# Kernel tuning notes

Hardware: AMD Instinct MI355X
Metric: run time of the kernel (lower is better)

The kernel has to match this reference:

```python
import jax, jax.numpy as jnp
import numpy as np

B, T, C, H = 2, 2048, 1024, 16


def setup_inputs() -> dict:
    key = jax.random.key(0)
    ks = jax.random.split(key, 9)
    s = 1.0 / np.sqrt(C)
    return {
        "query": jax.random.normal(ks[0], (B, T, C), dtype=jnp.float32),
        "Wq": jax.random.normal(ks[1], (C, C), dtype=jnp.float32) * s,
        "bq": jnp.zeros((C,), dtype=jnp.float32),
        "Wk": jax.random.normal(ks[2], (C, C), dtype=jnp.float32) * s,
        "bk": jnp.zeros((C,), dtype=jnp.float32),
        "Wv": jax.random.normal(ks[3], (C, C), dtype=jnp.float32) * s,
        "bv": jnp.zeros((C,), dtype=jnp.float32),
        "Wp": jax.random.normal(ks[4], (C, C), dtype=jnp.float32) * s,
        "bp": jnp.zeros((C,), dtype=jnp.float32),
        "n_head": H,
    }


def reference(query, Wq, bq, Wk, bk, Wv, bv, Wp, bp, n_head):
    b, t, c = query.shape
    d = c // n_head
    # QKV projections -> [b, h, t, d]
    q = (query @ Wq + bq).reshape(b, t, n_head, d).transpose(0, 2, 1, 3)
    k = (query @ Wk + bk).reshape(b, t, n_head, d).transpose(0, 2, 1, 3)
    v = (query @ Wv + bv).reshape(b, t, n_head, d).transpose(0, 2, 1, 3)
    scale = 1.0 / jnp.sqrt(jnp.asarray(d, dtype=query.dtype))
    att = jnp.einsum('bhtd,bhsd->bhts', q, k) * scale  # [b,h,t,t]
    causal = jnp.tril(jnp.ones((t, t), dtype=bool))
    att = jnp.where(causal[None, None, :, :], att, -jnp.inf)
    att = jax.nn.softmax(att, axis=-1)
    y = jnp.einsum('bhts,bhsd->bhtd', att, v)  # [b,h,t,d]
    y = y.transpose(0, 2, 1, 3).reshape(b, t, c)
    return y @ Wp + bp
```

## Files before the change

kernel.cpp:

```cpp
#include <hip/hip_runtime.h>
#include <math.h>

#define B_ 2
#define T_ 2048
#define C_ 1024
#define H_ 16
#define D_ 64
#define M_ (B_*T_)

typedef __bf16 bf16x8 __attribute__((ext_vector_type(8)));
typedef __bf16 bf16x4 __attribute__((ext_vector_type(4)));
typedef float  f32x4  __attribute__((ext_vector_type(4)));

__device__ __forceinline__ unsigned short f2bf(float f) {
    unsigned int u = __float_as_uint(f);
    u += 0x7FFFu + ((u >> 16) & 1u);
    return (unsigned short)(u >> 16);
}

__device__ __forceinline__ void gload16(const void* g, void* l) {
    __builtin_amdgcn_global_load_lds(
        (const __attribute__((address_space(1))) void*)g,
        (__attribute__((address_space(3))) void*)l, 16, 0, 0);
}

__global__ __launch_bounds__(256) void prep_kernel(
    const float* __restrict__ X, unsigned short* __restrict__ Xb,
    const float* __restrict__ W0, const float* __restrict__ W1,
    const float* __restrict__ W2, const float* __restrict__ W3,
    unsigned short* __restrict__ T0, unsigned short* __restrict__ T1,
    unsigned short* __restrict__ T2, unsigned short* __restrict__ T3)
{
    const int tid = threadIdx.x;
    if (blockIdx.x < 2048) {
        const size_t i = ((size_t)blockIdx.x * 256 + tid) * 8;
        const float4 a = *(const float4*)&X[i];
        const float4 b = *(const float4*)&X[i + 4];
        ushort4 s0, s1;
        s0.x = f2bf(a.x); s0.y = f2bf(a.y); s0.z = f2bf(a.z); s0.w = f2bf(a.w);
        s1.x = f2bf(b.x); s1.y = f2bf(b.y); s1.z = f2bf(b.z); s1.w = f2bf(b.w);
        *(ushort4*)&Xb[i]     = s0;
        *(ushort4*)&Xb[i + 4] = s1;
        return;
    }
    const int bz = blockIdx.x - 2048;
    const int z = bz >> 10, rem = bz & 1023;
    const float* W; unsigned short* Wt;
    switch (z) {
        case 0: W = W0; Wt = T0; break;
        case 1: W = W1; Wt = T1; break;
        case 2: W = W2; Wt = T2; break;
        default: W = W3; Wt = T3; break;
    }
    __shared__ unsigned short tile[32][33];
    const int k0 = (rem >> 5) * 32, n0 = (rem & 31) * 32;
    {
        const int r = tid >> 3, c = (tid & 7) * 4;
        const float4 v = *(const float4*)&W[(size_t)(k0 + r)*C_ + n0 + c];
        tile[c+0][r] = f2bf(v.x);
        tile[c+1][r] = f2bf(v.y);
        tile[c+2][r] = f2bf(v.z);
        tile[c+3][r] = f2bf(v.w);
    }
    __syncthreads();
    {
        const int r = tid >> 3, c = (tid & 7) * 4;
        ushort4 s;
        s.x = tile[r][c+0]; s.y = tile[r][c+1]; s.z = tile[r][c+2]; s.w = tile[r][c+3];
        *(ushort4*)&Wt[(size_t)(n0 + r)*C_ + k0 + c] = s;
    }
}

__global__ __launch_bounds__(256) void gemm_proj_kernel(
    const unsigned short* __restrict__ A, const unsigned short* __restrict__ Bt,
    const float* __restrict__ bias, float* __restrict__ out)
{
    __shared__ __align__(16) unsigned short Als[2][64 * 32];
    __shared__ __align__(16) unsigned short Bls[2][128 * 32];

    const int tid  = threadIdx.x;
    const int lane = tid & 63;
    const int wave = tid >> 6;
    const int wm = wave >> 1, wn = wave & 1;
    const int l15 = lane & 15, quad = lane >> 4;
    const int m0 = blockIdx.y * 64, n0 = blockIdx.x * 128;
    const int srow = lane >> 2;
    const int scol = (lane & 3) * 8;

    const f32x4 zero4 = {0.f, 0.f, 0.f, 0.f};
    f32x4 acc[2][4];
    #pragma unroll
    for (int i = 0; i < 2; ++i)
        #pragma unroll
        for (int j = 0; j < 4; ++j) acc[i][j] = zero4;

    for (int k0 = 0; k0 < C_; k0 += 64) {
        __syncthreads();
        #pragma unroll
        for (int h = 0; h < 2; ++h) {
            gload16(&A[(size_t)(m0 + wave*16 + srow)*C_ + k0 + h*32 + scol],
                    &Als[h][(wave*16)*32]);
            #pragma unroll
            for (int u = 0; u < 2; ++u) {
                const int r = wave*32 + u*16 + srow;
                gload16(&Bt[(size_t)(n0 + r)*C_ + k0 + h*32 + scol],
                        &Bls[h][(wave*32 + u*16)*32]);
            }
        }
        __syncthreads();

        #pragma unroll
        for (int h = 0; h < 2; ++h) {
            bf16x8 af[2], bfr[4];
            #pragma unroll
            for (int i = 0; i < 2; ++i)
                af[i] = *(const bf16x8*)&Als[h][(wm*32 + i*16 + l15)*32 + quad*8];
            #pragma unroll
            for (int j = 0; j < 4; ++j)
                bfr[j] = *(const bf16x8*)&Bls[h][(wn*64 + j*16 + l15)*32 + quad*8];

            #pragma unroll
            for (int i = 0; i < 2; ++i)
                #pragma unroll
                for (int j = 0; j < 4; ++j)
                    acc[i][j] = __builtin_amdgcn_mfma_f32_16x16x32_bf16(
                        af[i], bfr[j], acc[i][j], 0, 0, 0);
        }
    }

    #pragma unroll
    for (int j = 0; j < 4; ++j) {
        const int n = n0 + wn*64 + j*16 + l15;
        const float bv = bias[n];
        #pragma unroll
        for (int i = 0; i < 2; ++i)
            #pragma unroll
            for (int r = 0; r < 4; ++r) {
                const int m = m0 + wm*32 + i*16 + quad*4 + r;
                out[(size_t)m*C_ + n] = acc[i][j][r] + bv;
            }
    }
}

__global__ __launch_bounds__(512, 2) void gemm256_qkv_kernel(
    const unsigned short* __restrict__ A, const unsigned short* __restrict__ Bt,
    const float* __restrict__ b0, const float* __restrict__ b1,
    const float* __restrict__ b2,
    unsigned short* __restrict__ outq, unsigned short* __restrict__ outk,
    unsigned short* __restrict__ outv)
{
    __shared__ __align__(16) unsigned short lds[4 * 16384];

    const int tid  = threadIdx.x;
    const int lane = tid & 63;
    const int wave = tid >> 6;
    const int l15  = lane & 15, quad = lane >> 4;
    const int wm   = wave >> 2, wn = wave & 3;
    const int m0   = blockIdx.y * 256, n0 = blockIdx.x * 256;

    const int lrow = lane >> 2;
    const int csw  = ((lane & 3) ^ ((lane >> 3) & 3)) * 8;
    const int sw8  = (quad ^ ((l15 >> 1) & 3)) * 8;

#define STAGE(tt) do {                                                         \
        const int bi_ = ((tt) & 3) << 14;                                      \
        const int k0_ = (tt) << 5;                                             \
        const int ra_ = m0 + wave*32 + lrow;                                   \
        const int rb_ = n0 + wave*32 + lrow;                                   \
        gload16(&A [(size_t)ra_*C_ + k0_ + csw],      &lds[bi_ + wave*1024]);  \
        gload16(&Bt[(size_t)rb_*C_ + k0_ + csw],      &lds[bi_ + 8192 + wave*1024]); \
        gload16(&A [(size_t)(ra_+16)*C_ + k0_ + csw], &lds[bi_ + wave*1024 + 512]);  \
        gload16(&Bt[(size_t)(rb_+16)*C_ + k0_ + csw], &lds[bi_ + 8192 + wave*1024 + 512]); \
    } while (0)

    const f32x4 zero4 = {0.f, 0.f, 0.f, 0.f};
    f32x4 acc[8][4];
    #pragma unroll
    for (int i = 0; i < 8; ++i)
        #pragma unroll
        for (int j = 0; j < 4; ++j) acc[i][j] = zero4;

    STAGE(0); STAGE(1); STAGE(2);

    for (int t = 0; t < 32; ++t) {
        const int bi = (t & 3) << 14;
        __builtin_amdgcn_s_barrier();
        __builtin_amdgcn_sched_barrier(0);
        if (t < 29) {
            STAGE(t + 3);
            asm volatile("s_waitcnt vmcnt(12)" ::: "memory");
        } else if (t == 29) {
            asm volatile("s_waitcnt vmcnt(8)" ::: "memory");
        } else if (t == 30) {
            asm volatile("s_waitcnt vmcnt(4)" ::: "memory");
        } else {
            asm volatile("s_waitcnt vmcnt(0)" ::: "memory");
        }
        __builtin_amdgcn_s_barrier();
        __builtin_amdgcn_sched_barrier(0);

        const unsigned short* Ab = &lds[bi];
        const unsigned short* Bb = &lds[bi + 8192];

        bf16x8 bfr[4], af[4];
        #pragma unroll
        for (int j = 0; j < 4; ++j)
            bfr[j] = *(const bf16x8*)&Bb[(wn*64 + j*16 + l15)*32 + sw8];
        #pragma unroll
        for (int i = 0; i < 4; ++i)
            af[i] = *(const bf16x8*)&Ab[(wm*128 + i*16 + l15)*32 + sw8];

        __builtin_amdgcn_s_setprio(1);
        #pragma unroll
        for (int i = 0; i < 4; ++i)
            #pragma unroll
            for (int j = 0; j < 4; ++j)
                acc[i][j] = __builtin_amdgcn_mfma_f32_16x16x32_bf16(
                    af[i], bfr[j], acc[i][j], 0, 0, 0);
        __builtin_amdgcn_s_setprio(0);

        #pragma unroll
        for (int i = 0; i < 4; ++i)
            af[i] = *(const bf16x8*)&Ab[(wm*128 + 64 + i*16 + l15)*32 + sw8];

        __builtin_amdgcn_s_setprio(1);
        #pragma unroll
        for (int i = 0; i < 4; ++i)
            #pragma unroll
            for (int j = 0; j < 4; ++j)
                acc[4+i][j] = __builtin_amdgcn_mfma_f32_16x16x32_bf16(
                    af[i], bfr[j], acc[4+i][j], 0, 0, 0);
        __builtin_amdgcn_s_setprio(0);
    }
#undef STAGE

    __syncthreads();

    unsigned short* Ep = &lds[wave * 8192];
    const int which = n0 >> 10;
    const int c0 = (n0 & 1023) + wn * 64;
    const int h  = c0 >> 6;
    const int bb = m0 >> 11;
    const int t0 = (m0 & (T_ - 1)) + wm * 128;
    const int bh = bb * H_ + h;
    const float* bp = (which == 0) ? b0 : (which == 1 ? b1 : b2);
    const float qscale = (which == 0) ? 0.18033688f : 1.0f;

    if (which < 2) {
        __bf16* Eb = (__bf16*)Ep;
        #pragma unroll
        for (int j = 0; j < 4; ++j) {
            const int cl = j*16 + l15;
            const float bias = bp[c0 + cl];
            #pragma unroll
            for (int i = 0; i < 8; ++i)
                #pragma unroll
                for (int r = 0; r < 4; ++r)
                    Eb[(i*16 + quad*4 + r)*64 + cl] =
                        (__bf16)((acc[i][j][r] + bias) * qscale);
        }
        unsigned short* op = (which == 0) ? outq : outk;
        const int row8 = lane >> 3, chunk = lane & 7;
        #pragma unroll
        for (int u = 0; u < 16; ++u) {
            const int row = u*8 + row8;
            const uint4 v = *(const uint4*)&Ep[row*64 + chunk*8];
            *(uint4*)&op[((size_t)bh*T_ + t0 + row)*D_ + chunk*8] = v;
        }
    } else {
        #pragma unroll
        for (int j = 0; j < 4; ++j) {
            const int cl = j*16 + l15;
            const float bias = bp[c0 + cl];
            const int xo = (cl & 7) * 8;
            #pragma unroll
            for (int i = 0; i < 8; ++i) {
                bf16x4 pk = {(__bf16)(acc[i][j][0] + bias),
                             (__bf16)(acc[i][j][1] + bias),
                             (__bf16)(acc[i][j][2] + bias),
                             (__bf16)(acc[i][j][3] + bias)};
                *(bf16x4*)&Ep[cl*128 + ((i*16 + quad*4) ^ xo)] = pk;
            }
        }
        const int d4 = lane >> 4, chunk = lane & 15;
        #pragma unroll
        for (int u = 0; u < 16; ++u) {
            const int d = u*4 + d4;
            const uint4 v = *(const uint4*)&Ep[d*128 + ((chunk*8) ^ ((d & 7)*8))];
            *(uint4*)&outv[((size_t)bh*D_ + d)*T_ + t0 + chunk*8] = v;
        }
    }
}

__global__ __launch_bounds__(256) void flash_mfma_kernel(
    const unsigned short* __restrict__ Qs, const unsigned short* __restrict__ Ks,
    const unsigned short* __restrict__ Vts, unsigned short* __restrict__ Y,
    float* __restrict__ parts, float* __restrict__ lbase)
{
    __shared__ __align__(16) unsigned short Kls[64 * 64];
    __shared__ __align__(16) unsigned short Vls[64 * 64];
    __shared__ __align__(16) unsigned short Pls[4 * 2048];

    const int tid  = threadIdx.x;
    const int lane = tid & 63, wave = tid >> 6;
    const int l15  = lane & 15, quad = lane >> 4;
    const int job  = blockIdx.x >> 5;
    const int bh   = blockIdx.x & 31;
    const bool isA = (job < 8);
    const int a    = isA ? job : job - 8;

    int qts[2], slos[2], shis[2], slots[2], nseg;
    if (isA) {
        qts[0] = a;      slos[0] = 0;        shis[0] = 2*a + 2;  slots[0] = -1;
        qts[1] = 15 - a; slos[1] = 0;        shis[1] = 15 - 2*a; slots[1] = 0;
        nseg = 2;
    } else {
        qts[0] = 15 - a; slos[0] = 15 - 2*a; shis[0] = 32 - 2*a; slots[0] = 1;
        nseg = 1;
    }

    unsigned short* Pw = &Pls[wave * 2048];
    const int kd_s = wave >> 1;
    const int c8_s = (kd_s * 4 + quad) * 8;
    const int b_ = bh >> 4, h_ = bh & (H_ - 1);
    const f32x4 zero4 = {0.f, 0.f, 0.f, 0.f};

    for (int sg = 0; sg < nseg; ++sg) {
        const int qt  = qts[sg];
        const int qw0 = qt * 128 + wave * 32;

        bf16x8 qf[2][2];
        #pragma unroll
        for (int i = 0; i < 2; ++i)
            #pragma unroll
            for (int kd = 0; kd < 2; ++kd)
                qf[i][kd] = *(const bf16x8*)&Qs[((size_t)bh*T_ + qw0 + i*16 + l15)*D_
                                                + kd*32 + quad*8];

        f32x4 o[2][4];
        #pragma unroll
        for (int i = 0; i < 2; ++i)
            #pragma unroll
            for (int jd = 0; jd < 4; ++jd) o[i][jd] = zero4;
        float lsum[2] = {0.f, 0.f};

        for (int it = slos[sg]; it < shis[sg]; ++it) {
            const int s0 = it * 64;
            __syncthreads();
            #pragma unroll
            for (int u = 0; u < 2; ++u) {
                const int cu  = 2*wave + u;
                const int row = ((cu & 3) << 4) + l15;
                gload16(&Ks [((size_t)bh*T_ + s0 + row)*D_ + c8_s],
                        (char*)Kls + cu*1024);
                gload16(&Vts[((size_t)bh*D_ + row)*T_ + s0 + c8_s],
                        (char*)Vls + cu*1024);
            }
            __syncthreads();

            if (s0 > qw0 + 31) continue;

            f32x4 st[2][4];
            #pragma unroll
            for (int i = 0; i < 2; ++i)
                #pragma unroll
                for (int j = 0; j < 4; ++j) st[i][j] = zero4;
            #pragma unroll
            for (int kd = 0; kd < 2; ++kd) {
                bf16x8 kf[4];
                #pragma unroll
                for (int j = 0; j < 4; ++j)
                    kf[j] = *(const bf16x8*)&Kls[lane*8 + j*512 + kd*2048];
                #pragma unroll
                for (int i = 0; i < 2; ++i)
                    #pragma unroll
                    for (int j = 0; j < 4; ++j)
                        st[i][j] = __builtin_amdgcn_mfma_f32_16x16x32_bf16(
                            kf[j], qf[i][kd], st[i][j], 0, 0, 0);
            }

            const bool diag = (s0 + 63 > qw0);
            #pragma unroll
            for (int i = 0; i < 2; ++i) {
                const int qrow = qw0 + i*16 + l15;
                #pragma unroll
                for (int j = 0; j < 4; ++j)
                    #pragma unroll
                    for (int r = 0; r < 4; ++r) {
                        float e = __builtin_amdgcn_exp2f(st[i][j][r]);
                        if (diag && (s0 + j*16 + quad*4 + r > qrow)) e = 0.f;
                        st[i][j][r] = e;
                        lsum[i] += e;
                    }
            }

            #pragma unroll
            for (int i = 0; i < 2; ++i)
                #pragma unroll
                for (int j = 0; j < 4; ++j) {
                    bf16x4 pk = {(__bf16)st[i][j][0], (__bf16)st[i][j][1],
                                 (__bf16)st[i][j][2], (__bf16)st[i][j][3]};
                    *(bf16x4*)&Pw[(((j>>1)*2 + i)*4 + (j&1)*2 + (quad>>1))*128
                                   + l15*8 + (quad&1)*4] = pk;
                }

            #pragma unroll
            for (int kk = 0; kk < 2; ++kk) {
                bf16x8 pf[2], vf[4];
                #pragma unroll
                for (int i = 0; i < 2; ++i)
                    pf[i] = *(const bf16x8*)&Pw[(kk*2 + i)*512 + lane*8];
                #pragma unroll
                for (int jd = 0; jd < 4; ++jd)
                    vf[jd] = *(const bf16x8*)&Vls[lane*8 + jd*512 + kk*2048];
                #pragma unroll
                for (int i = 0; i < 2; ++i)
                    #pragma unroll
                    for (int jd = 0; jd < 4; ++jd)
                        o[i][jd] = __builtin_amdgcn_mfma_f32_16x16x32_bf16(
                            vf[jd], pf[i], o[i][jd], 0, 0, 0);
            }
        }

        #pragma unroll
        for (int i = 0; i < 2; ++i) {
            float v = lsum[i];
            v += __shfl_xor(v, 16, 64);
            v += __shfl_xor(v, 32, 64);
            lsum[i] = v;
        }

        if (slots[sg] < 0) {
            #pragma unroll
            for (int i = 0; i < 2; ++i) {
                const float inv = 1.0f / lsum[i];
                const int t = qw0 + i*16 + l15;
                #pragma unroll
                for (int jd = 0; jd < 4; ++jd) {
                    bf16x4 pk = {(__bf16)(o[i][jd][0] * inv),
                                 (__bf16)(o[i][jd][1] * inv),
                                 (__bf16)(o[i][jd][2] * inv),
                                 (__bf16)(o[i][jd][3] * inv)};
                    *(bf16x4*)&Y[((size_t)(b_*T_ + t))*C_ + h_*D_ + jd*16 + quad*4]
                        = pk;
                }
            }
        } else {
            const int gpi = bh*16 + a*2 + slots[sg];
            float* Op = parts + (size_t)gpi*8192;
            float* Lp = lbase + gpi*128;
            #pragma unroll
            for (int i = 0; i < 2; ++i) {
                const int tl = wave*32 + i*16 + l15;
                if (quad == 0) Lp[tl] = lsum[i];
                #pragma unroll
                for (int jd = 0; jd < 4; ++jd)
                    *(f32x4*)&Op[(size_t)tl*64 + jd*16 + quad*4] = o[i][jd];
            }
        }
    }
}

__global__ __launch_bounds__(256) void merge_kernel(
    const float* __restrict__ parts, const float* __restrict__ lbase,
    unsigned short* __restrict__ Y)
{
    const int pair = blockIdx.x;
    const int bh = pair >> 3, p = pair & 7;
    const int qt = 15 - p;
    const int g0 = bh*16 + p*2;
    const float* O0 = parts + (size_t)g0*8192;
    const float* O1 = O0 + 8192;
    const float* L0 = lbase + g0*128;
    const float* L1 = L0 + 128;

    const int tid = threadIdx.x;
    const int r = tid >> 1, c0 = (tid & 1) * 32;
    const float inv = 1.0f / (L0[r] + L1[r]);
    const int b = bh >> 4, h = bh & (H_ - 1);
    const int t = qt*128 + r;
    #pragma unroll
    for (int k = 0; k < 8; ++k) {
        const f32x4 a  = *(const f32x4*)&O0[(size_t)r*64 + c0 + k*4];
        const f32x4 bb = *(const f32x4*)&O1[(size_t)r*64 + c0 + k*4];
        bf16x4 pk = {(__bf16)((a[0]+bb[0])*inv), (__bf16)((a[1]+bb[1])*inv),
                     (__bf16)((a[2]+bb[2])*inv), (__bf16)((a[3]+bb[3])*inv)};
        *(bf16x4*)&Y[((size_t)(b*T_ + t))*C_ + h*D_ + c0 + k*4] = pk;
    }
}

extern "C" void kernel_launch(void* const* d_in, const int* in_sizes, int n_in,
                              void* d_out, int out_size, void* d_ws, size_t ws_size,
                              hipStream_t stream) {
    const float* query = (const float*)d_in[0];
    const float* Wq = (const float*)d_in[1];
    const float* bq = (const float*)d_in[2];
    const float* Wk = (const float*)d_in[3];
    const float* bk = (const float*)d_in[4];
    const float* Wv = (const float*)d_in[5];
    const float* bv = (const float*)d_in[6];
    const float* Wp = (const float*)d_in[7];
    const float* bp = (const float*)d_in[8];
    float* out = (float*)d_out;

    char* ws = (char*)d_ws;
    unsigned short* qbf   = (unsigned short*)(ws);
    unsigned short* kbf   = (unsigned short*)(ws + 8388608);
    unsigned short* vtbf  = (unsigned short*)(ws + 16777216);
    unsigned short* WtP   = (unsigned short*)(ws + 25165824);
    unsigned short* WtQKV = (unsigned short*)(ws + 27262976);
    unsigned short* yb    = (unsigned short*)(ws + 33554432);
    unsigned short* qx    = (unsigned short*)(ws + 41943040);
    float* lbase = (float*)(ws + 27262976);
    float* parts = out;

    prep_kernel<<<6144, 256, 0, stream>>>(
        query, qx, Wq, Wk, Wv, Wp,
        WtQKV, WtQKV + (size_t)C_*C_, WtQKV + 2*(size_t)C_*C_, WtP);

    gemm256_qkv_kernel<<<dim3(12, 16), 512, 0, stream>>>(
        qx, WtQKV, bq, bk, bv, qbf, kbf, vtbf);

    flash_mfma_kernel<<<512, 256, 0, stream>>>(qbf, kbf, vtbf, yb, parts, lbase);
    merge_kernel<<<256, 256, 0, stream>>>(parts, lbase, yb);

    gemm_proj_kernel<<<dim3(C_/128, M_/64), 256, 0, stream>>>(
        yb, WtP, bp, out);
}
```

Before: 197.2 us.

## Split KV tiles across two wave groups per block with LDS merge

```diff
diff --git a/kernel.cpp b/kernel.cpp
--- a/kernel.cpp
+++ b/kernel.cpp
@@ -292,17 +292,17 @@
     }
 }
 
-__global__ __launch_bounds__(256) void flash_mfma_kernel(
+__global__ __launch_bounds__(512) void flash_mfma_kernel(
     const unsigned short* __restrict__ Qs, const unsigned short* __restrict__ Ks,
     const unsigned short* __restrict__ Vts, unsigned short* __restrict__ Y,
     float* __restrict__ parts, float* __restrict__ lbase)
 {
-    __shared__ __align__(16) unsigned short Kls[64 * 64];
-    __shared__ __align__(16) unsigned short Vls[64 * 64];
-    __shared__ __align__(16) unsigned short Pls[4 * 2048];
+    __shared__ __align__(16) unsigned short lds[2 * 16384];
 
     const int tid  = threadIdx.x;
     const int lane = tid & 63, wave = tid >> 6;
+    const int grp  = wave >> 2;
+    const int w4   = wave & 3;
     const int l15  = lane & 15, quad = lane >> 4;
     const int job  = blockIdx.x >> 5;
     const int bh   = blockIdx.x & 31;
@@ -319,15 +319,21 @@
         nseg = 1;
     }
 
-    unsigned short* Pw = &Pls[wave * 2048];
-    const int kd_s = wave >> 1;
+    unsigned short* Kls = &lds[grp * 16384];
+    unsigned short* Vls = Kls + 4096;
+    unsigned short* Pg  = Kls + 8192;
+    unsigned short* Pw  = Pg + w4 * 2048;
+    float* Osc = (float*)&lds[16384];
+    float* Lsc = (float*)&lds[8192];
+
+    const int kd_s = w4 >> 1;
     const int c8_s = (kd_s * 4 + quad) * 8;
     const int b_ = bh >> 4, h_ = bh & (H_ - 1);
     const f32x4 zero4 = {0.f, 0.f, 0.f, 0.f};
 
     for (int sg = 0; sg < nseg; ++sg) {
         const int qt  = qts[sg];
-        const int qw0 = qt * 128 + wave * 32;
+        const int qw0 = qt * 128 + w4 * 32;
 
         bf16x8 qf[2][2];
         #pragma unroll
@@ -344,21 +350,29 @@
             for (int jd = 0; jd < 4; ++jd) o[i][jd] = zero4;
         float lsum[2] = {0.f, 0.f};
 
-        for (int it = slos[sg]; it < shis[sg]; ++it) {
-            const int s0 = it * 64;
+        const int lo = slos[sg], nj = shis[sg] - slos[sg];
+        const int njj = (nj + 1) >> 1;
+
+        for (int jj = 0; jj < njj; ++jj) {
+            const int itg = 2*jj + grp;
+            const bool valid = (itg < nj);
+            const int s0 = (lo + itg) * 64;
+
             __syncthreads();
-            #pragma unroll
-            for (int u = 0; u < 2; ++u) {
-                const int cu  = 2*wave + u;
-                const int row = ((cu & 3) << 4) + l15;
-                gload16(&Ks [((size_t)bh*T_ + s0 + row)*D_ + c8_s],
-                        (char*)Kls + cu*1024);
-                gload16(&Vts[((size_t)bh*D_ + row)*T_ + s0 + c8_s],
-                        (char*)Vls + cu*1024);
+            if (valid) {
+                #pragma unroll
+                for (int u = 0; u < 2; ++u) {
+                    const int cu  = 2*w4 + u;
+                    const int row = ((cu & 3) << 4) + l15;
+                    gload16(&Ks [((size_t)bh*T_ + s0 + row)*D_ + c8_s],
+                            (char*)Kls + cu*1024);
+                    gload16(&Vts[((size_t)bh*D_ + row)*T_ + s0 + c8_s],
+                            (char*)Vls + cu*1024);
+                }
             }
             __syncthreads();
 
-            if (s0 > qw0 + 31) continue;
+            if (!valid || s0 > qw0 + 31) continue;
 
             f32x4 st[2][4];
             #pragma unroll
@@ -430,32 +444,55 @@
             lsum[i] = v;
         }
 
-        if (slots[sg] < 0) {
+        __syncthreads();
+        if (grp == 1) {
             #pragma unroll
             for (int i = 0; i < 2; ++i) {
-                const float inv = 1.0f / lsum[i];
-                const int t = qw0 + i*16 + l15;
-                #pragma unroll
-                for (int jd = 0; jd < 4; ++jd) {
-                    bf16x4 pk = {(__bf16)(o[i][jd][0] * inv),
-                                 (__bf16)(o[i][jd][1] * inv),
-                                 (__bf16)(o[i][jd][2] * inv),
-                                 (__bf16)(o[i][jd][3] * inv)};
-                    *(bf16x4*)&Y[((size_t)(b_*T_ + t))*C_ + h_*D_ + jd*16 + quad*4]
-                        = pk;
+                const int tl = w4*32 + i*16 + l15;
+                if (quad == 0) Lsc[tl] = lsum[i];
+                #pragma unroll
+                for (int jd = 0; jd < 4; ++jd)
+                    *(f32x4*)&Osc[(size_t)tl*64 + jd*16 + quad*4] = o[i][jd];
+            }
+        }
+        __syncthreads();
+        if (grp == 0) {
+            #pragma unroll
+            for (int i = 0; i < 2; ++i) {
+                const int tl = w4*32 + i*16 + l15;
+                lsum[i] += Lsc[tl];
+                #pragma unroll
+                for (int jd = 0; jd < 4; ++jd)
+                    o[i][jd] += *(const f32x4*)&Osc[(size_t)tl*64 + jd*16 + quad*4];
+            }
+
+            if (slots[sg] < 0) {
+                #pragma unroll
+                for (int i = 0; i < 2; ++i) {
+                    const float inv = 1.0f / lsum[i];
+                    const int t = qw0 + i*16 + l15;
+                    #pragma unroll
+                    for (int jd = 0; jd < 4; ++jd) {
+                        bf16x4 pk = {(__bf16)(o[i][jd][0] * inv),
+                                     (__bf16)(o[i][jd][1] * inv),
+                                     (__bf16)(o[i][jd][2] * inv),
+                                     (__bf16)(o[i][jd][3] * inv)};
+                        *(bf16x4*)&Y[((size_t)(b_*T_ + t))*C_ + h_*D_ + jd*16 + quad*4]
+                            = pk;
+                    }
                 }
-            }
-        } else {
-            const int gpi = bh*16 + a*2 + slots[sg];
-            float* Op = parts + (size_t)gpi*8192;
-            float* Lp = lbase + gpi*128;
-            #pragma unroll
-            for (int i = 0; i < 2; ++i) {
-                const int tl = wave*32 + i*16 + l15;
-                if (quad == 0) Lp[tl] = lsum[i];
-                #pragma unroll
-                for (int jd = 0; jd < 4; ++jd)
-                    *(f32x4*)&Op[(size_t)tl*64 + jd*16 + quad*4] = o[i][jd];
+            } else {
+                const int gpi = bh*16 + a*2 + slots[sg];
+                float* Op = parts + (size_t)gpi*8192;
+                float* Lp = lbase + gpi*128;
+                #pragma unroll
+                for (int i = 0; i < 2; ++i) {
+                    const int tl = w4*32 + i*16 + l15;
+                    if (quad == 0) Lp[tl] = lsum[i];
+                    #pragma unroll
+                    for (int jd = 0; jd < 4; ++jd)
+                        *(f32x4*)&Op[(size_t)tl*64 + jd*16 + quad*4] = o[i][jd];
+                }
             }
         }
     }
@@ -521,7 +558,7 @@
     gemm256_qkv_kernel<<<dim3(12, 16), 512, 0, stream>>>(
         qx, WtQKV, bq, bk, bv, qbf, kbf, vtbf);
 
-    flash_mfma_kernel<<<512, 256, 0, stream>>>(qbf, kbf, vtbf, yb, parts, lbase);
+    flash_mfma_kernel<<<512, 512, 0, stream>>>(qbf, kbf, vtbf, yb, parts, lbase);
     merge_kernel<<<256, 256, 0, stream>>>(parts, lbase, yb);
 
     gemm_proj_kernel<<<dim3(C_/128, M_/64), 256, 0, stream>>>(
```

Measured after the change: 207.9 us. +5.4%, slower.

## Halve flash-attention query tile to 64 rows and double grid size

Applied to the files above, without the earlier changes.

```diff
diff --git a/kernel.cpp b/kernel.cpp
--- a/kernel.cpp
+++ b/kernel.cpp
@@ -306,16 +306,16 @@
     const int l15  = lane & 15, quad = lane >> 4;
     const int job  = blockIdx.x >> 5;
     const int bh   = blockIdx.x & 31;
-    const bool isA = (job < 8);
-    const int a    = isA ? job : job - 8;
+    const bool isA = (job < 16);
+    const int a    = job & 15;
 
     int qts[2], slos[2], shis[2], slots[2], nseg;
     if (isA) {
-        qts[0] = a;      slos[0] = 0;        shis[0] = 2*a + 2;  slots[0] = -1;
-        qts[1] = 15 - a; slos[1] = 0;        shis[1] = 15 - 2*a; slots[1] = 0;
+        qts[0] = a;      slos[0] = 0;      shis[0] = a + 1;  slots[0] = -1;
+        qts[1] = 31 - a; slos[1] = 0;      shis[1] = 16 - a; slots[1] = 0;
         nseg = 2;
     } else {
-        qts[0] = 15 - a; slos[0] = 15 - 2*a; shis[0] = 32 - 2*a; slots[0] = 1;
+        qts[0] = 31 - a; slos[0] = 16 - a; shis[0] = 32 - a; slots[0] = 1;
         nseg = 1;
     }
 
@@ -327,22 +327,18 @@
 
     for (int sg = 0; sg < nseg; ++sg) {
         const int qt  = qts[sg];
-        const int qw0 = qt * 128 + wave * 32;
-
-        bf16x8 qf[2][2];
-        #pragma unroll
-        for (int i = 0; i < 2; ++i)
-            #pragma unroll
-            for (int kd = 0; kd < 2; ++kd)
-                qf[i][kd] = *(const bf16x8*)&Qs[((size_t)bh*T_ + qw0 + i*16 + l15)*D_
-                                                + kd*32 + quad*8];
-
-        f32x4 o[2][4];
-        #pragma unroll
-        for (int i = 0; i < 2; ++i)
-            #pragma unroll
-            for (int jd = 0; jd < 4; ++jd) o[i][jd] = zero4;
-        float lsum[2] = {0.f, 0.f};
+        const int qw0 = qt * 64 + wave * 16;
+
+        bf16x8 qf[2];
+        #pragma unroll
+        for (int kd = 0; kd < 2; ++kd)
+            qf[kd] = *(const bf16x8*)&Qs[((size_t)bh*T_ + qw0 + l15)*D_
+                                          + kd*32 + quad*8];
+
+        f32x4 o[4];
+        #pragma unroll
+        for (int jd = 0; jd < 4; ++jd) o[jd] = zero4;
+        float lsum = 0.f;
 
         for (int it = slos[sg]; it < shis[sg]; ++it) {
             const int s0 = it * 64;
@@ -358,13 +354,11 @@
             }
             __syncthreads();
 
-            if (s0 > qw0 + 31) continue;
-
-            f32x4 st[2][4];
-            #pragma unroll
-            for (int i = 0; i < 2; ++i)
-                #pragma unroll
-                for (int j = 0; j < 4; ++j) st[i][j] = zero4;
+            if (s0 > qw0 + 15) continue;
+
+            f32x4 st[4];
+            #pragma unroll
+            for (int j = 0; j < 4; ++j) st[j] = zero4;
             #pragma unroll
             for (int kd = 0; kd < 2; ++kd) {
                 bf16x8 kf[4];
@@ -372,91 +366,73 @@
                 for (int j = 0; j < 4; ++j)
                     kf[j] = *(const bf16x8*)&Kls[lane*8 + j*512 + kd*2048];
                 #pragma unroll
-                for (int i = 0; i < 2; ++i)
-                    #pragma unroll
-                    for (int j = 0; j < 4; ++j)
-                        st[i][j] = __builtin_amdgcn_mfma_f32_16x16x32_bf16(
-                            kf[j], qf[i][kd], st[i][j], 0, 0, 0);
+                for (int j = 0; j < 4; ++j)
+                    st[j] = __builtin_amdgcn_mfma_f32_16x16x32_bf16(
+                        kf[j], qf[kd], st[j], 0, 0, 0);
             }
 
             const bool diag = (s0 + 63 > qw0);
-            #pragma unroll
-            for (int i = 0; i < 2; ++i) {
-                const int qrow = qw0 + i*16 + l15;
-                #pragma unroll
-                for (int j = 0; j < 4; ++j)
-                    #pragma unroll
-                    for (int r = 0; r < 4; ++r) {
-                        float e = __builtin_amdgcn_exp2f(st[i][j][r]);
-                        if (diag && (s0 + j*16 + quad*4 + r > qrow)) e = 0.f;
-                        st[i][j][r] = e;
-                        lsum[i] += e;
-                    }
-            }
-
-            #pragma unroll
-            for (int i = 0; i < 2; ++i)
-                #pragma unroll
-                for (int j = 0; j < 4; ++j) {
-                    bf16x4 pk = {(__bf16)st[i][j][0], (__bf16)st[i][j][1],
-                                 (__bf16)st[i][j][2], (__bf16)st[i][j][3]};
-                    *(bf16x4*)&Pw[(((j>>1)*2 + i)*4 + (j&1)*2 + (quad>>1))*128
-                                   + l15*8 + (quad&1)*4] = pk;
+            const int qrow = qw0 + l15;
+            #pragma unroll
+            for (int j = 0; j < 4; ++j)
+                #pragma unroll
+                for (int r = 0; r < 4; ++r) {
+                    float e = __builtin_amdgcn_exp2f(st[j][r]);
+                    if (diag && (s0 + j*16 + quad*4 + r > qrow)) e = 0.f;
+                    st[j][r] = e;
+                    lsum += e;
                 }
 
             #pragma unroll
+            for (int j = 0; j < 4; ++j) {
+                bf16x4 pk = {(__bf16)st[j][0], (__bf16)st[j][1],
+                             (__bf16)st[j][2], (__bf16)st[j][3]};
+                *(bf16x4*)&Pw[((j>>1)*8 + (j&1)*2 + (quad>>1))*128
+                               + l15*8 + (quad&1)*4] = pk;
+            }
+
+            #pragma unroll
             for (int kk = 0; kk < 2; ++kk) {
-                bf16x8 pf[2], vf[4];
-                #pragma unroll
-                for (int i = 0; i < 2; ++i)
-                    pf[i] = *(const bf16x8*)&Pw[(kk*2 + i)*512 + lane*8];
+                bf16x8 pf = *(const bf16x8*)&Pw[(kk*2)*512 + lane*8];
+                bf16x8 vf[4];
                 #pragma unroll
                 for (int jd = 0; jd < 4; ++jd)
                     vf[jd] = *(const bf16x8*)&Vls[lane*8 + jd*512 + kk*2048];
                 #pragma unroll
-                for (int i = 0; i < 2; ++i)
-                    #pragma unroll
-                    for (int jd = 0; jd < 4; ++jd)
-                        o[i][jd] = __builtin_amdgcn_mfma_f32_16x16x32_bf16(
-                            vf[jd], pf[i], o[i][jd], 0, 0, 0);
-            }
-        }
-
-        #pragma unroll
-        for (int i = 0; i < 2; ++i) {
-            float v = lsum[i];
+                for (int jd = 0; jd < 4; ++jd)
+                    o[jd] = __builtin_amdgcn_mfma_f32_16x16x32_bf16(
+                        vf[jd], pf, o[jd], 0, 0, 0);
+            }
+        }
+
+        {
+            float v = lsum;
             v += __shfl_xor(v, 16, 64);
             v += __shfl_xor(v, 32, 64);
-            lsum[i] = v;
+            lsum = v;
         }
 
         if (slots[sg] < 0) {
-            #pragma unroll
-            for (int i = 0; i < 2; ++i) {
-                const float inv = 1.0f / lsum[i];
-                const int t = qw0 + i*16 + l15;
-                #pragma unroll
-                for (int jd = 0; jd < 4; ++jd) {
-                    bf16x4 pk = {(__bf16)(o[i][jd][0] * inv),
-                                 (__bf16)(o[i][jd][1] * inv),
-                                 (__bf16)(o[i][jd][2] * inv),
-                                 (__bf16)(o[i][jd][3] * inv)};
-                    *(bf16x4*)&Y[((size_t)(b_*T_ + t))*C_ + h_*D_ + jd*16 + quad*4]
-                        = pk;
-                }
+            const float inv = 1.0f / lsum;
+            const int t = qw0 + l15;
+            #pragma unroll
+            for (int jd = 0; jd < 4; ++jd) {
+                bf16x4 pk = {(__bf16)(o[jd][0] * inv),
+                             (__bf16)(o[jd][1] * inv),
+                             (__bf16)(o[jd][2] * inv),
+                             (__bf16)(o[jd][3] * inv)};
+                *(bf16x4*)&Y[((size_t)(b_*T_ + t))*C_ + h_*D_ + jd*16 + quad*4]
+                    = pk;
             }
         } else {
-            const int gpi = bh*16 + a*2 + slots[sg];
-            float* Op = parts + (size_t)gpi*8192;
-            float* Lp = lbase + gpi*128;
-            #pragma unroll
-            for (int i = 0; i < 2; ++i) {
-                const int tl = wave*32 + i*16 + l15;
-                if (quad == 0) Lp[tl] = lsum[i];
-                #pragma unroll
-                for (int jd = 0; jd < 4; ++jd)
-                    *(f32x4*)&Op[(size_t)tl*64 + jd*16 + quad*4] = o[i][jd];
-            }
+            const int gpi = bh*32 + a*2 + slots[sg];
+            float* Op = parts + (size_t)gpi*4096;
+            float* Lp = lbase + gpi*64;
+            const int tl = wave*16 + l15;
+            if (quad == 0) Lp[tl] = lsum;
+            #pragma unroll
+            for (int jd = 0; jd < 4; ++jd)
+                *(f32x4*)&Op[(size_t)tl*64 + jd*16 + quad*4] = o[jd];
         }
     }
 }
@@ -466,21 +442,21 @@
     unsigned short* __restrict__ Y)
 {
     const int pair = blockIdx.x;
-    const int bh = pair >> 3, p = pair & 7;
-    const int qt = 15 - p;
-    const int g0 = bh*16 + p*2;
-    const float* O0 = parts + (size_t)g0*8192;
-    const float* O1 = O0 + 8192;
-    const float* L0 = lbase + g0*128;
-    const float* L1 = L0 + 128;
+    const int bh = pair >> 4, p = pair & 15;
+    const int qt = 31 - p;
+    const int g0 = bh*32 + p*2;
+    const float* O0 = parts + (size_t)g0*4096;
+    const float* O1 = O0 + 4096;
+    const float* L0 = lbase + g0*64;
+    const float* L1 = L0 + 64;
 
     const int tid = threadIdx.x;
-    const int r = tid >> 1, c0 = (tid & 1) * 32;
+    const int r = tid >> 2, c0 = (tid & 3) * 16;
     const float inv = 1.0f / (L0[r] + L1[r]);
     const int b = bh >> 4, h = bh & (H_ - 1);
-    const int t = qt*128 + r;
+    const int t = qt*64 + r;
     #pragma unroll
-    for (int k = 0; k < 8; ++k) {
+    for (int k = 0; k < 4; ++k) {
         const f32x4 a  = *(const f32x4*)&O0[(size_t)r*64 + c0 + k*4];
         const f32x4 bb = *(const f32x4*)&O1[(size_t)r*64 + c0 + k*4];
         bf16x4 pk = {(__bf16)((a[0]+bb[0])*inv), (__bf16)((a[1]+bb[1])*inv),
@@ -521,8 +497,8 @@
     gemm256_qkv_kernel<<<dim3(12, 16), 512, 0, stream>>>(
         qx, WtQKV, bq, bk, bv, qbf, kbf, vtbf);
 
-    flash_mfma_kernel<<<512, 256, 0, stream>>>(qbf, kbf, vtbf, yb, parts, lbase);
-    merge_kernel<<<256, 256, 0, stream>>>(parts, lbase, yb);
+    flash_mfma_kernel<<<1024, 256, 0, stream>>>(qbf, kbf, vtbf, yb, parts, lbase);
+    merge_kernel<<<512, 256, 0, stream>>>(parts, lbase, yb);
 
     gemm_proj_kernel<<<dim3(C_/128, M_/64), 256, 0, stream>>>(
         yb, WtP, bp, out);
```

New measurement: 190.4 us. -3.5%, faster.

## Switch flash attention to 32x32x16 MFMA with register-resident P via permlane swap

Applied to the files above, without the earlier changes.

```diff
diff --git a/kernel.cpp b/kernel.cpp
--- a/kernel.cpp
+++ b/kernel.cpp
@@ -11,11 +11,19 @@
 typedef __bf16 bf16x8 __attribute__((ext_vector_type(8)));
 typedef __bf16 bf16x4 __attribute__((ext_vector_type(4)));
 typedef float  f32x4  __attribute__((ext_vector_type(4)));
+typedef float  f32x16 __attribute__((ext_vector_type(16)));
 
 __device__ __forceinline__ unsigned short f2bf(float f) {
     unsigned int u = __float_as_uint(f);
     u += 0x7FFFu + ((u >> 16) & 1u);
     return (unsigned short)(u >> 16);
+}
+
+__device__ __forceinline__ bf16x8 pack4(unsigned a, unsigned b,
+                                        unsigned c, unsigned d) {
+    union { unsigned u[4]; bf16x8 v; } t;
+    t.u[0] = a; t.u[1] = b; t.u[2] = c; t.u[3] = d;
+    return t.v;
 }
 
 __device__ __forceinline__ void gload16(const void* g, void* l) {
@@ -299,11 +307,13 @@
 {
     __shared__ __align__(16) unsigned short Kls[64 * 64];
     __shared__ __align__(16) unsigned short Vls[64 * 64];
-    __shared__ __align__(16) unsigned short Pls[4 * 2048];
+    __shared__ float lsums[4][32];
 
     const int tid  = threadIdx.x;
     const int lane = tid & 63, wave = tid >> 6;
-    const int l15  = lane & 15, quad = lane >> 4;
+    const int krl  = lane & 31, hi = lane >> 5;
+    const int srow8 = lane >> 3;
+    const int schk8 = ((lane & 7) ^ srow8) * 8;
     const int job  = blockIdx.x >> 5;
     const int bh   = blockIdx.x & 31;
     const bool isA = (job < 8);
@@ -319,146 +329,138 @@
         nseg = 1;
     }
 
-    unsigned short* Pw = &Pls[wave * 2048];
-    const int kd_s = wave >> 1;
-    const int c8_s = (kd_s * 4 + quad) * 8;
     const int b_ = bh >> 4, h_ = bh & (H_ - 1);
-    const f32x4 zero4 = {0.f, 0.f, 0.f, 0.f};
+
+#define FSTAGE(itv) do {                                                       \
+        const int s0_ = (itv) * 64;                                            \
+        const int cu0_ = 2*wave, cu1_ = 2*wave + 1;                            \
+        const int r0_ = cu0_*8 + srow8, r1_ = cu1_*8 + srow8;                  \
+        gload16(&Ks [((size_t)bh*T_ + s0_ + r0_)*D_ + schk8],                  \
+                (char*)Kls + cu0_*1024);                                       \
+        gload16(&Vts[((size_t)bh*D_ + r0_)*T_ + s0_ + schk8],                  \
+                (char*)Vls + cu0_*1024);                                       \
+        gload16(&Ks [((size_t)bh*T_ + s0_ + r1_)*D_ + schk8],                  \
+                (char*)Kls + cu1_*1024);                                       \
+        gload16(&Vts[((size_t)bh*D_ + r1_)*T_ + s0_ + schk8],                  \
+                (char*)Vls + cu1_*1024);                                       \
+    } while (0)
 
     for (int sg = 0; sg < nseg; ++sg) {
         const int qt  = qts[sg];
         const int qw0 = qt * 128 + wave * 32;
-
-        bf16x8 qf[2][2];
-        #pragma unroll
-        for (int i = 0; i < 2; ++i)
-            #pragma unroll
-            for (int kd = 0; kd < 2; ++kd)
-                qf[i][kd] = *(const bf16x8*)&Qs[((size_t)bh*T_ + qw0 + i*16 + l15)*D_
-                                                + kd*32 + quad*8];
-
-        f32x4 o[2][4];
-        #pragma unroll
-        for (int i = 0; i < 2; ++i)
-            #pragma unroll
-            for (int jd = 0; jd < 4; ++jd) o[i][jd] = zero4;
-        float lsum[2] = {0.f, 0.f};
+        const int qrow = qw0 + krl;
+
+        bf16x8 qf[4];
+        #pragma unroll
+        for (int ds = 0; ds < 4; ++ds)
+            qf[ds] = *(const bf16x8*)&Qs[((size_t)bh*T_ + qrow)*D_ + ds*16 + hi*8];
+
+        f32x16 o[2];
+        #pragma unroll
+        for (int dt = 0; dt < 2; ++dt)
+            #pragma unroll
+            for (int r = 0; r < 16; ++r) o[dt][r] = 0.f;
+        float lsum = 0.f;
 
         for (int it = slos[sg]; it < shis[sg]; ++it) {
             const int s0 = it * 64;
             __syncthreads();
-            #pragma unroll
-            for (int u = 0; u < 2; ++u) {
-                const int cu  = 2*wave + u;
-                const int row = ((cu & 3) << 4) + l15;
-                gload16(&Ks [((size_t)bh*T_ + s0 + row)*D_ + c8_s],
-                        (char*)Kls + cu*1024);
-                gload16(&Vts[((size_t)bh*D_ + row)*T_ + s0 + c8_s],
-                        (char*)Vls + cu*1024);
-            }
+            FSTAGE(it);
             __syncthreads();
 
             if (s0 > qw0 + 31) continue;
 
-            f32x4 st[2][4];
-            #pragma unroll
-            for (int i = 0; i < 2; ++i)
-                #pragma unroll
-                for (int j = 0; j < 4; ++j) st[i][j] = zero4;
-            #pragma unroll
-            for (int kd = 0; kd < 2; ++kd) {
-                bf16x8 kf[4];
-                #pragma unroll
-                for (int j = 0; j < 4; ++j)
-                    kf[j] = *(const bf16x8*)&Kls[lane*8 + j*512 + kd*2048];
-                #pragma unroll
-                for (int i = 0; i < 2; ++i)
-                    #pragma unroll
-                    for (int j = 0; j < 4; ++j)
-                        st[i][j] = __builtin_amdgcn_mfma_f32_16x16x32_bf16(
-                            kf[j], qf[i][kd], st[i][j], 0, 0, 0);
+            f32x16 st[2];
+            #pragma unroll
+            for (int kt = 0; kt < 2; ++kt)
+                #pragma unroll
+                for (int r = 0; r < 16; ++r) st[kt][r] = 0.f;
+            #pragma unroll
+            for (int kt = 0; kt < 2; ++kt) {
+                #pragma unroll
+                for (int ds = 0; ds < 4; ++ds) {
+                    const int row = kt*32 + krl;
+                    bf16x8 kf = *(const bf16x8*)
+                        &Kls[row*64 + (((ds*2 + hi) ^ (krl & 7)) << 3)];
+                    st[kt] = __builtin_amdgcn_mfma_f32_32x32x16_bf16(
+                        kf, qf[ds], st[kt], 0, 0, 0);
+                }
             }
 
             const bool diag = (s0 + 63 > qw0);
             #pragma unroll
-            for (int i = 0; i < 2; ++i) {
-                const int qrow = qw0 + i*16 + l15;
-                #pragma unroll
-                for (int j = 0; j < 4; ++j)
-                    #pragma unroll
-                    for (int r = 0; r < 4; ++r) {
-                        float e = __builtin_amdgcn_exp2f(st[i][j][r]);
-                        if (diag && (s0 + j*16 + quad*4 + r > qrow)) e = 0.f;
-                        st[i][j][r] = e;
-                        lsum[i] += e;
-                    }
-            }
-
-            #pragma unroll
-            for (int i = 0; i < 2; ++i)
-                #pragma unroll
-                for (int j = 0; j < 4; ++j) {
-                    bf16x4 pk = {(__bf16)st[i][j][0], (__bf16)st[i][j][1],
-                                 (__bf16)st[i][j][2], (__bf16)st[i][j][3]};
-                    *(bf16x4*)&Pw[(((j>>1)*2 + i)*4 + (j&1)*2 + (quad>>1))*128
-                                   + l15*8 + (quad&1)*4] = pk;
+            for (int kt = 0; kt < 2; ++kt) {
+                const int kb = s0 + kt*32 + 4*hi;
+                #pragma unroll
+                for (int reg = 0; reg < 16; ++reg) {
+                    const int crow = (reg & 3) + 8*(reg >> 2);
+                    float e = __builtin_amdgcn_exp2f(st[kt][reg]);
+                    if (diag && (kb + crow > qrow)) e = 0.f;
+                    st[kt][reg] = e;
+                    lsum += e;
                 }
-
-            #pragma unroll
-            for (int kk = 0; kk < 2; ++kk) {
-                bf16x8 pf[2], vf[4];
-                #pragma unroll
-                for (int i = 0; i < 2; ++i)
-                    pf[i] = *(const bf16x8*)&Pw[(kk*2 + i)*512 + lane*8];
-                #pragma unroll
-                for (int jd = 0; jd < 4; ++jd)
-                    vf[jd] = *(const bf16x8*)&Vls[lane*8 + jd*512 + kk*2048];
-                #pragma unroll
-                for (int i = 0; i < 2; ++i)
-                    #pragma unroll
-                    for (int jd = 0; jd < 4; ++jd)
-                        o[i][jd] = __builtin_amdgcn_mfma_f32_16x16x32_bf16(
-                            vf[jd], pf[i], o[i][jd], 0, 0, 0);
-            }
-        }
-
-        #pragma unroll
-        for (int i = 0; i < 2; ++i) {
-            float v = lsum[i];
-            v += __shfl_xor(v, 16, 64);
-            v += __shfl_xor(v, 32, 64);
-            lsum[i] = v;
-        }
+            }
+
+            bf16x8 pa[4];
+            #pragma unroll
+            for (int kt = 0; kt < 2; ++kt) {
+                #pragma unroll
+                for (int hh = 0; hh < 2; ++hh) {
+                    const int rb = hh * 8;
+                    unsigned c0, c1, c2, c3;
+                    asm("v_cvt_pk_bf16_f32 %0, %1, %2"
+                        : "=v"(c0) : "v"(st[kt][rb+0]), "v"(st[kt][rb+1]));
+                    asm("v_cvt_pk_bf16_f32 %0, %1, %2"
+                        : "=v"(c1) : "v"(st[kt][rb+2]), "v"(st[kt][rb+3]));
+                    asm("v_cvt_pk_bf16_f32 %0, %1, %2"
+                        : "=v"(c2) : "v"(st[kt][rb+4]), "v"(st[kt][rb+5]));
+                    asm("v_cvt_pk_bf16_f32 %0, %1, %2"
+                        : "=v"(c3) : "v"(st[kt][rb+6]), "v"(st[kt][rb+7]));
+                    asm("v_permlane32_swap_b32 %0, %1" : "+v"(c0), "+v"(c2));
+                    asm("v_permlane32_swap_b32 %0, %1" : "+v"(c1), "+v"(c3));
+                    pa[kt*2 + hh] = pack4(c0, c1, c2, c3);
+                }
+            }
+
+            #pragma unroll
+            for (int dt = 0; dt < 2; ++dt) {
+                #pragma unroll
+                for (int ks = 0; ks < 4; ++ks) {
+                    const int rowd = dt*32 + krl;
+                    bf16x8 vb = *(const bf16x8*)
+                        &Vls[rowd*64 + (((ks*2 + hi) ^ (krl & 7)) << 3)];
+                    o[dt] = __builtin_amdgcn_mfma_f32_32x32x16_bf16(
+                        pa[ks], vb, o[dt], 0, 0, 0);
+                }
+            }
+        }
+
+        lsum += __shfl_xor(lsum, 32, 64);
+        if (lane < 32) lsums[wave][krl] = lsum;
 
         if (slots[sg] < 0) {
             #pragma unroll
-            for (int i = 0; i < 2; ++i) {
-                const float inv = 1.0f / lsum[i];
-                const int t = qw0 + i*16 + l15;
-                #pragma unroll
-                for (int jd = 0; jd < 4; ++jd) {
-                    bf16x4 pk = {(__bf16)(o[i][jd][0] * inv),
-                                 (__bf16)(o[i][jd][1] * inv),
-                                 (__bf16)(o[i][jd][2] * inv),
-                                 (__bf16)(o[i][jd][3] * inv)};
-                    *(bf16x4*)&Y[((size_t)(b_*T_ + t))*C_ + h_*D_ + jd*16 + quad*4]
-                        = pk;
-                }
+            for (int reg = 0; reg < 16; ++reg) {
+                const int q = (reg & 3) + 8*(reg >> 2) + 4*hi;
+                const float inv = 1.0f / lsums[wave][q];
+                const size_t yb = ((size_t)(b_*T_ + qw0 + q))*C_ + h_*D_;
+                *(__bf16*)&Y[yb + krl]      = (__bf16)(o[0][reg] * inv);
+                *(__bf16*)&Y[yb + 32 + krl] = (__bf16)(o[1][reg] * inv);
             }
         } else {
             const int gpi = bh*16 + a*2 + slots[sg];
             float* Op = parts + (size_t)gpi*8192;
             float* Lp = lbase + gpi*128;
-            #pragma unroll
-            for (int i = 0; i < 2; ++i) {
-                const int tl = wave*32 + i*16 + l15;
-                if (quad == 0) Lp[tl] = lsum[i];
-                #pragma unroll
-                for (int jd = 0; jd < 4; ++jd)
-                    *(f32x4*)&Op[(size_t)tl*64 + jd*16 + quad*4] = o[i][jd];
-            }
-        }
-    }
+            if (lane < 32) Lp[wave*32 + lane] = lsum;
+            #pragma unroll
+            for (int reg = 0; reg < 16; ++reg) {
+                const int tl = wave*32 + (reg & 3) + 8*(reg >> 2) + 4*hi;
+                Op[(size_t)tl*64 + krl]      = o[0][reg];
+                Op[(size_t)tl*64 + 32 + krl] = o[1][reg];
+            }
+        }
+    }
+#undef FSTAGE
 }
 
 __global__ __launch_bounds__(256) void merge_kernel(
```

Result: faster. 190.1 us (-3.6%).
